# Optimization experiments

Hardware: AMD Instinct MI355X
Metric: run time of the kernel (lower is better)

## Reference

```python
import jax, jax.numpy as jnp
import numpy as np

N, D = 8192, 256
ALPHA, BETA, K = 50.0, 1.0, 2


def setup_inputs() -> dict:
    key = jax.random.key(0)
    k1, k2, k3, k4 = jax.random.split(key, 4)
    Q = jax.random.normal(k1, (N, D), dtype=jnp.float32)
    # 0/1 similarity structure; diagonal forced nonzero so no row is fully masked
    sim = jax.random.randint(k2, (N, N), 0, 2).astype(jnp.float32)
    sim = sim.at[jnp.arange(N), jnp.arange(N)].set(1.0)
    # nn.Linear(in_dim, in_dim) params: y = x @ W.T + b
    bound = 1.0 / np.sqrt(D)
    W = jax.random.uniform(k3, (D, D), jnp.float32, -bound, bound)
    b = jax.random.uniform(k4, (D,), jnp.float32, -bound, bound)
    return {"Q": Q, "sim_mat": sim, "W": W, "b": b}


def reference(Q, sim_mat, W, b):
    mask = sim_mat == 0  # (N, N) bool, constant across iterations
    H = Q
    for _ in range(K):
        H_proj = H @ W.T + b                      # (N, d)
        scores = H_proj @ H_proj.T                # (N, N)
        scores = jnp.where(mask, -jnp.inf, scores)
        lamb = jax.nn.softmax(scores, axis=1)     # (N, N)
        numerator = ALPHA * Q + BETA * (lamb @ H)
        denominator = ALPHA + BETA * jnp.sum(lamb, axis=1, keepdims=True)
        H = numerator / denominator
    return H
```

## Files before the change

kernel.cpp:

```cpp
#include <hip/hip_runtime.h>
#include <hip/hip_bf16.h>

#define NN 8192
#define DD 256
#define ALPHA 50.0f
#define BETA 1.0f
#define THR 10.0f
#define KQ 8
#define KEYS (NN / KQ)
#define STEPS (KEYS / 32)
#define QROWS 64

typedef __attribute__((ext_vector_type(8))) short short8;
typedef __attribute__((ext_vector_type(4))) float f32x4;

static __device__ __forceinline__ ushort f2bf(float f) {
    union { __hip_bfloat16 h; ushort u; } v;
    v.h = __float2bfloat16(f);
    return v.u;
}
static __device__ __forceinline__ float bf2f(ushort u) {
    union { unsigned u; float f; } v; v.u = ((unsigned)u) << 16;
    return v.f;
}
static __device__ __forceinline__ void gl_lds16(const ushort* g, ushort* l) {
    __builtin_amdgcn_global_load_lds(
        (const __attribute__((address_space(1))) unsigned int*)g,
        (__attribute__((address_space(3))) unsigned int*)l, 16, 0, 0);
}

__global__ void k_wconv(const float* __restrict__ W, ushort* __restrict__ Wb) {
    int i = blockIdx.x * 256 + threadIdx.x;
    Wb[i] = f2bf(W[i]);
}

__global__ __launch_bounds__(256) void k_pack(const float* __restrict__ sim,
                                              unsigned* __restrict__ bits) {
    __shared__ unsigned char nibs[256];
    int row = blockIdx.x;
    int tid = threadIdx.x;
    for (int p = 0; p < 8; ++p) {
        int col = p * 1024 + tid * 4;
        float4 v = *reinterpret_cast<const float4*>(sim + (size_t)row * NN + col);
        unsigned char nib = (unsigned char)((v.x != 0.f) | ((v.y != 0.f) << 1) |
                                            ((v.z != 0.f) << 2) | ((v.w != 0.f) << 3));
        nibs[tid] = nib;
        __syncthreads();
        if (tid < 32) {
            unsigned word = 0;
#pragma unroll
            for (int i = 0; i < 8; ++i) word |= ((unsigned)nibs[tid * 8 + i]) << (4 * i);
            bits[row * (NN / 32) + p * 32 + tid] = word;
        }
        __syncthreads();
    }
}

__global__ __launch_bounds__(256) void k_convert(const float* __restrict__ H,
                                                 ushort* __restrict__ Hv,
                                                 ushort* __restrict__ Hvt) {
    __shared__ ushort T[64][72];
    int tile = blockIdx.x;
    int r0 = (tile >> 2) * 64;
    int c0 = (tile & 3) * 64;
    int tid = threadIdx.x;
    int tr = tid >> 4;
    int tc = (tid & 15) * 4;
    for (int i = 0; i < 4; ++i) {
        int r = tr + i * 16;
        float4 v = *reinterpret_cast<const float4*>(H + (size_t)(r0 + r) * DD + c0 + tc);
        ushort4 o;
        o.x = f2bf(v.x); o.y = f2bf(v.y); o.z = f2bf(v.z); o.w = f2bf(v.w);
        *reinterpret_cast<ushort4*>(Hv + (size_t)(r0 + r) * DD + c0 + tc) = o;
        T[tc + 0][r] = o.x; T[tc + 1][r] = o.y; T[tc + 2][r] = o.z; T[tc + 3][r] = o.w;
    }
    __syncthreads();
    for (int i = 0; i < 4; ++i) {
        int c = tr + i * 16;
        ushort4 o;
        o.x = T[c][tc + 0]; o.y = T[c][tc + 1]; o.z = T[c][tc + 2]; o.w = T[c][tc + 3];
        *reinterpret_cast<ushort4*>(Hvt + (size_t)(c0 + c) * NN + r0 + tc) = o;
    }
}

__global__ __launch_bounds__(256) void k_proj(const ushort* __restrict__ Hv,
                                              const ushort* __restrict__ Wb,
                                              const float* __restrict__ b,
                                              ushort* __restrict__ Hp) {
    int w = threadIdx.x >> 6;
    int lane = threadIdx.x & 63;
    int row0 = (blockIdx.x >> 1) * 64 + w * 16;
    int ch = blockIdx.x & 1;
    int lr = lane & 15;
    int lk = lane >> 4;
    short8 af[8];
    for (int kk = 0; kk < 8; ++kk)
        af[kk] = *reinterpret_cast<const short8*>(Hv + (size_t)(row0 + lr) * DD + kk * 32 + lk * 8);
    for (int t = 0; t < 8; ++t) {
        f32x4 acc = {0.f, 0.f, 0.f, 0.f};
        int col = (ch * 8 + t) * 16 + lr;
        for (int kk = 0; kk < 8; ++kk) {
            short8 bf = *reinterpret_cast<const short8*>(Wb + (size_t)col * DD + kk * 32 + lk * 8);
            acc = __builtin_amdgcn_mfma_f32_16x16x32_bf16(af[kk], bf, acc, 0, 0, 0);
        }
        float bias = b[col];
        for (int j = 0; j < 4; ++j) {
            int row = row0 + lk * 4 + j;
            Hp[(size_t)row * DD + col] = f2bf(acc[j] + bias);
        }
    }
}

#define PSTR 40
#define SMEM_ATTN (2 * 32 * 256 * 2 + 2 * 256 * 32 * 2 + 4 * 16 * PSTR * 2)
__global__ __launch_bounds__(256) void k_attn(const ushort* __restrict__ Hp,
                                              const ushort* __restrict__ Hvt,
                                              const unsigned* __restrict__ bits,
                                              ushort* __restrict__ Opart,
                                              float* __restrict__ mpart,
                                              float* __restrict__ lpart) {
    extern __shared__ char smem[];
    ushort* KlB = (ushort*)smem;
    ushort* VlB = (ushort*)(smem + 32768);
    ushort* Pl  = (ushort*)(smem + 65536);

    const int tid = threadIdx.x;
    const int w = tid >> 6;
    const int lane = tid & 63;
    const int lr = lane & 15;
    const int lk = lane >> 4;
    const int bid = blockIdx.x;
    const int kq = bid & 7;
    const int qt = bid >> 3;
    const int rw0 = qt * QROWS + w * 16;
    const int kstart = kq * KEYS;

    int kSrc[4], vSrc[4], dstO[4];
#pragma unroll
    for (int i = 0; i < 4; ++i) {
        int S = (w * 4 + i) * 64 + lane;
        int rK = S >> 5, cpK = S & 31;
        kSrc[i] = rK * 256 + (cpK ^ (rK & 7)) * 8;
        int rV = S >> 2, cpV = S & 3;
        vSrc[i] = rV * NN + (cpV ^ ((rV >> 2) & 3)) * 8;
        dstO[i] = S * 8;
    }
    auto stageK = [&](int buf, int kb) {
        const ushort* Kg = Hp + (size_t)kb * DD;
        ushort* base = KlB + buf * (32 * 256);
#pragma unroll
        for (int i = 0; i < 4; ++i) gl_lds16(Kg + kSrc[i], base + dstO[i]);
    };
    auto stageV = [&](int buf, int kb) {
        const ushort* Vg = Hvt + kb;
        ushort* base = VlB + buf * (256 * 32);
#pragma unroll
        for (int i = 0; i < 4; ++i) gl_lds16(Vg + vSrc[i], base + dstO[i]);
    };

    int Koff[8];
#pragma unroll
    for (int kk = 0; kk < 8; ++kk)
        Koff[kk] = (lr << 9) + ((((kk << 2) + lk) ^ (lr & 7)) << 4);
    const int vBase = (lr << 6) + ((lk ^ ((lr >> 2) & 3)) << 4);

    short8 qf[8];
#pragma unroll
    for (int kk = 0; kk < 8; ++kk)
        qf[kk] = *reinterpret_cast<const short8*>(Hp + (size_t)(rw0 + lr) * DD + kk * 32 + lk * 8);

    f32x4 o[17];
#pragma unroll
    for (int t = 0; t < 17; ++t) o[t] = {0.f, 0.f, 0.f, 0.f};
    float m[4] = {-1e30f, -1e30f, -1e30f, -1e30f};

    short8 ones;
#pragma unroll
    for (int e = 0; e < 8; ++e) ones[e] = (short)0x3f80;

    stageK(0, kstart);
    stageV(0, kstart);
    __syncthreads();

    const int rowbase = (rw0 + lk * 4) * (NN / 32);
    ushort* Pw = Pl + (size_t)w * 16 * PSTR;
    int cur = 0;
    for (int step = 0; step < STEPS; ++step) {
        const int kb = kstart + step * 32;
        if (step + 1 < STEPS) {
            stageK(cur ^ 1, kb + 32);
            stageV(cur ^ 1, kb + 32);
        }
        const int wi = kb >> 5;
        unsigned mwj[4];
#pragma unroll
        for (int j = 0; j < 4; ++j) mwj[j] = bits[rowbase + j * (NN / 32) + wi];

        const char* Kb = (const char*)(KlB + cur * (32 * 256));
        f32x4 s0 = {0.f, 0.f, 0.f, 0.f}, s1 = {0.f, 0.f, 0.f, 0.f};
        __builtin_amdgcn_s_setprio(1);
#pragma unroll
        for (int kk = 0; kk < 8; ++kk) {
            short8 k0 = *reinterpret_cast<const short8*>(Kb + Koff[kk]);
            short8 k1 = *reinterpret_cast<const short8*>(Kb + Koff[kk] + (16 << 9));
            s0 = __builtin_amdgcn_mfma_f32_16x16x32_bf16(qf[kk], k0, s0, 0, 0, 0);
            s1 = __builtin_amdgcn_mfma_f32_16x16x32_bf16(qf[kk], k1, s1, 0, 0, 0);
        }
        __builtin_amdgcn_s_setprio(0);
        float c = -1e30f;
#pragma unroll
        for (int j = 0; j < 4; ++j) {
            float a0 = ((mwj[j] >> lr) & 1u) ? s0[j] : -1e30f;
            float a1 = ((mwj[j] >> (lr + 16)) & 1u) ? s1[j] : -1e30f;
            s0[j] = a0; s1[j] = a1;
            c = fmaxf(c, fmaxf(a0, a1) - m[j]);
        }
        if (__any(c > THR)) {
#pragma unroll
            for (int j = 0; j < 4; ++j) {
                float mx = fmaxf(s0[j], s1[j]);
                mx = fmaxf(mx, __shfl_xor(mx, 1));
                mx = fmaxf(mx, __shfl_xor(mx, 2));
                mx = fmaxf(mx, __shfl_xor(mx, 4));
                mx = fmaxf(mx, __shfl_xor(mx, 8));
                float mn = fmaxf(m[j], mx);
                float scale = __expf(m[j] - mn);
                m[j] = mn;
#pragma unroll
                for (int t = 0; t < 17; ++t) o[t][j] *= scale;
            }
        }
#pragma unroll
        for (int j = 0; j < 4; ++j) {
            Pw[(lk * 4 + j) * PSTR + lr]      = f2bf(__expf(s0[j] - m[j]));
            Pw[(lk * 4 + j) * PSTR + 16 + lr] = f2bf(__expf(s1[j] - m[j]));
        }
        asm volatile("s_waitcnt lgkmcnt(0)" ::: "memory");
        __builtin_amdgcn_sched_barrier(0);
        short8 pa = *reinterpret_cast<const short8*>(Pw + lr * PSTR + lk * 8);
        const char* Vb = (const char*)(VlB + cur * (256 * 32));
        __builtin_amdgcn_s_setprio(1);
#pragma unroll
        for (int t = 0; t < 16; ++t) {
            short8 vf = *reinterpret_cast<const short8*>(Vb + vBase + (t << 10));
            o[t] = __builtin_amdgcn_mfma_f32_16x16x32_bf16(pa, vf, o[t], 0, 0, 0);
        }
        o[16] = __builtin_amdgcn_mfma_f32_16x16x32_bf16(pa, ones, o[16], 0, 0, 0);
        __builtin_amdgcn_s_setprio(0);
        __syncthreads();
        cur ^= 1;
    }

    ushort* op = Opart + ((size_t)kq * NN + rw0) * DD;
#pragma unroll
    for (int t = 0; t < 16; ++t)
#pragma unroll
        for (int j = 0; j < 4; ++j)
            op[(size_t)(lk * 4 + j) * DD + t * 16 + lr] = f2bf(o[t][j]);
    if (lr == 0) {
#pragma unroll
        for (int j = 0; j < 4; ++j) {
            mpart[kq * NN + rw0 + lk * 4 + j] = m[j];
            lpart[kq * NN + rw0 + lk * 4 + j] = o[16][j];
        }
    }
}

__global__ __launch_bounds__(256) void k_merge8(const ushort* __restrict__ Opart,
                                                const float* __restrict__ mpart,
                                                const float* __restrict__ lpart,
                                                const float* __restrict__ Qo,
                                                float* __restrict__ dst) {
    int w = threadIdx.x >> 6;
    int lane = threadIdx.x & 63;
    int r0 = blockIdx.x * 32 + w * 8;
    for (int rr = 0; rr < 8; ++rr) {
        int r = r0 + rr;
        float mv[8], f[8];
        float M = -1e30f;
#pragma unroll
        for (int p = 0; p < 8; ++p) { mv[p] = mpart[p * NN + r]; M = fmaxf(M, mv[p]); }
        float L = 0.f;
#pragma unroll
        for (int p = 0; p < 8; ++p) { f[p] = __expf(mv[p] - M); L += f[p] * lpart[p * NN + r]; }
        float invL = 1.0f / L;
        int c = lane * 4;
        float a0 = 0.f, a1 = 0.f, a2 = 0.f, a3 = 0.f;
#pragma unroll
        for (int p = 0; p < 8; ++p) {
            ushort4 u = *reinterpret_cast<const ushort4*>(Opart + ((size_t)p * NN + r) * DD + c);
            a0 += f[p] * bf2f(u.x); a1 += f[p] * bf2f(u.y);
            a2 += f[p] * bf2f(u.z); a3 += f[p] * bf2f(u.w);
        }
        float4 qv = *reinterpret_cast<const float4*>(Qo + (size_t)r * DD + c);
        float4 ov;
        ov.x = (ALPHA * qv.x + a0 * invL) * (1.0f / (ALPHA + BETA));
        ov.y = (ALPHA * qv.y + a1 * invL) * (1.0f / (ALPHA + BETA));
        ov.z = (ALPHA * qv.z + a2 * invL) * (1.0f / (ALPHA + BETA));
        ov.w = (ALPHA * qv.w + a3 * invL) * (1.0f / (ALPHA + BETA));
        *reinterpret_cast<float4*>(dst + (size_t)r * DD + c) = ov;
    }
}

extern "C" void kernel_launch(void* const* d_in, const int* in_sizes, int n_in,
                              void* d_out, int out_size, void* d_ws, size_t ws_size,
                              hipStream_t stream) {
    const float* Q   = (const float*)d_in[0];
    const float* sim = (const float*)d_in[1];
    const float* W   = (const float*)d_in[2];
    const float* b   = (const float*)d_in[3];
    float* out = (float*)d_out;

    char* ws = (char*)d_ws;
    size_t off = 0;
    ushort* Hv   = (ushort*)(ws + off); off += (size_t)NN * DD * 2;
    ushort* HvtA = (ushort*)(ws + off); off += (size_t)NN * DD * 2;
    ushort* HvtB = (ushort*)(ws + off); off += (size_t)NN * DD * 2;
    ushort* Hp   = (ushort*)(ws + off); off += (size_t)NN * DD * 2;
    ushort* Wb   = (ushort*)(ws + off); off += (size_t)DD * DD * 2;
    unsigned* bits = (unsigned*)(ws + off); off += (size_t)NN * (NN / 32) * 4;
    float*  H1   = (float*)(ws + off);  off += (size_t)NN * DD * 4;
    ushort* Opart = (ushort*)(ws + off); off += (size_t)KQ * NN * DD * 2;
    float*  mpart = (float*)(ws + off);  off += (size_t)KQ * NN * 4;
    float*  lpart = (float*)(ws + off);  off += (size_t)KQ * NN * 4;

    (void)hipFuncSetAttribute((const void*)k_attn,
                              hipFuncAttributeMaxDynamicSharedMemorySize, SMEM_ATTN);

    k_wconv<<<DD * DD / 256, 256, 0, stream>>>(W, Wb);
    k_pack<<<NN, 256, 0, stream>>>(sim, bits);
    k_convert<<<(NN / 64) * (DD / 64), 256, 0, stream>>>(Q, Hv, HvtA);

    k_proj<<<NN / 32, 256, 0, stream>>>(Hv, Wb, b, Hp);
    k_attn<<<(NN / QROWS) * KQ, 256, SMEM_ATTN, stream>>>(Hp, HvtA, bits, Opart, mpart, lpart);
    k_merge8<<<NN / 32, 256, 0, stream>>>(Opart, mpart, lpart, Q, H1);
    k_convert<<<(NN / 64) * (DD / 64), 256, 0, stream>>>(H1, Hv, HvtB);

    k_proj<<<NN / 32, 256, 0, stream>>>(Hv, Wb, b, Hp);
    k_attn<<<(NN / QROWS) * KQ, 256, SMEM_ATTN, stream>>>(Hp, HvtB, bits, Opart, mpart, lpart);
    k_merge8<<<NN / 32, 256, 0, stream>>>(Opart, mpart, lpart, Q, out);
}
```

Baseline: 354.7 us.

## Use 8-wave attention blocks with triple-buffered K/V and LDS-staged mask bits

```diff
diff --git a/kernel.cpp b/kernel.cpp
--- a/kernel.cpp
+++ b/kernel.cpp
@@ -9,7 +9,7 @@
 #define KQ 8
 #define KEYS (NN / KQ)
 #define STEPS (KEYS / 32)
-#define QROWS 64
+#define QROWS 128
 
 typedef __attribute__((ext_vector_type(8))) short short8;
 typedef __attribute__((ext_vector_type(4))) float f32x4;
@@ -23,7 +23,7 @@
     union { unsigned u; float f; } v; v.u = ((unsigned)u) << 16;
     return v.f;
 }
-static __device__ __forceinline__ void gl_lds16(const ushort* g, ushort* l) {
+static __device__ __forceinline__ void gl_lds16(const void* g, void* l) {
     __builtin_amdgcn_global_load_lds(
         (const __attribute__((address_space(1))) unsigned int*)g,
         (__attribute__((address_space(3))) unsigned int*)l, 16, 0, 0);
@@ -112,8 +112,12 @@
 }
 
 #define PSTR 40
-#define SMEM_ATTN (2 * 32 * 256 * 2 + 2 * 256 * 32 * 2 + 4 * 16 * PSTR * 2)
-__global__ __launch_bounds__(256) void k_attn(const ushort* __restrict__ Hp,
+#define KBYTES (32 * 256 * 2)
+#define VBYTES (256 * 32 * 2)
+#define PBYTES (8 * 16 * PSTR * 2)
+#define BBYTES (QROWS * 32 * 4)
+#define SMEM_ATTN (3 * KBYTES + 3 * VBYTES + PBYTES + BBYTES)
+__global__ __launch_bounds__(512) void k_attn(const ushort* __restrict__ Hp,
                                               const ushort* __restrict__ Hvt,
                                               const unsigned* __restrict__ bits,
                                               ushort* __restrict__ Opart,
@@ -121,8 +125,9 @@
                                               float* __restrict__ lpart) {
     extern __shared__ char smem[];
     ushort* KlB = (ushort*)smem;
-    ushort* VlB = (ushort*)(smem + 32768);
-    ushort* Pl  = (ushort*)(smem + 65536);
+    ushort* VlB = (ushort*)(smem + 3 * KBYTES);
+    ushort* Pl  = (ushort*)(smem + 3 * KBYTES + 3 * VBYTES);
+    unsigned* Bl = (unsigned*)(smem + 3 * KBYTES + 3 * VBYTES + PBYTES);
 
     const int tid = threadIdx.x;
     const int w = tid >> 6;
@@ -135,10 +140,10 @@
     const int rw0 = qt * QROWS + w * 16;
     const int kstart = kq * KEYS;
 
-    int kSrc[4], vSrc[4], dstO[4];
-#pragma unroll
-    for (int i = 0; i < 4; ++i) {
-        int S = (w * 4 + i) * 64 + lane;
+    int kSrc[2], vSrc[2], dstO[2];
+#pragma unroll
+    for (int i = 0; i < 2; ++i) {
+        int S = i * 512 + tid;
         int rK = S >> 5, cpK = S & 31;
         kSrc[i] = rK * 256 + (cpK ^ (rK & 7)) * 8;
         int rV = S >> 2, cpV = S & 3;
@@ -149,13 +154,13 @@
         const ushort* Kg = Hp + (size_t)kb * DD;
         ushort* base = KlB + buf * (32 * 256);
 #pragma unroll
-        for (int i = 0; i < 4; ++i) gl_lds16(Kg + kSrc[i], base + dstO[i]);
+        for (int i = 0; i < 2; ++i) gl_lds16(Kg + kSrc[i], base + dstO[i]);
     };
     auto stageV = [&](int buf, int kb) {
         const ushort* Vg = Hvt + kb;
         ushort* base = VlB + buf * (256 * 32);
 #pragma unroll
-        for (int i = 0; i < 4; ++i) gl_lds16(Vg + vSrc[i], base + dstO[i]);
+        for (int i = 0; i < 2; ++i) gl_lds16(Vg + vSrc[i], base + dstO[i]);
     };
 
     int Koff[8];
@@ -178,23 +183,37 @@
 #pragma unroll
     for (int e = 0; e < 8; ++e) ones[e] = (short)0x3f80;
 
+    {
+        const unsigned* Bg = bits + (size_t)(qt * QROWS) * (NN / 32) + kq * 32;
+#pragma unroll
+        for (int i = 0; i < 2; ++i) {
+            int S = i * 512 + tid;
+            int r = S >> 3, c = S & 7;
+            gl_lds16(Bg + (size_t)r * (NN / 32) + c * 4, Bl + S * 4);
+        }
+    }
     stageK(0, kstart);
     stageV(0, kstart);
-    __syncthreads();
-
-    const int rowbase = (rw0 + lk * 4) * (NN / 32);
+    stageK(1, kstart + 32);
+    stageV(1, kstart + 32);
+    asm volatile("s_waitcnt vmcnt(4)" ::: "memory");
+    __builtin_amdgcn_s_barrier();
+    __builtin_amdgcn_sched_barrier(0);
+
     ushort* Pw = Pl + (size_t)w * 16 * PSTR;
+    const int mrow = (w * 16 + lk * 4) * 32;
     int cur = 0;
     for (int step = 0; step < STEPS; ++step) {
         const int kb = kstart + step * 32;
-        if (step + 1 < STEPS) {
-            stageK(cur ^ 1, kb + 32);
-            stageV(cur ^ 1, kb + 32);
-        }
-        const int wi = kb >> 5;
+        const bool staged = (step + 2 < STEPS);
+        if (staged) {
+            int nb = cur + 2; if (nb >= 3) nb -= 3;
+            stageK(nb, kb + 64);
+            stageV(nb, kb + 64);
+        }
         unsigned mwj[4];
 #pragma unroll
-        for (int j = 0; j < 4; ++j) mwj[j] = bits[rowbase + j * (NN / 32) + wi];
+        for (int j = 0; j < 4; ++j) mwj[j] = Bl[mrow + j * 32 + step];
 
         const char* Kb = (const char*)(KlB + cur * (32 * 256));
         f32x4 s0 = {0.f, 0.f, 0.f, 0.f}, s1 = {0.f, 0.f, 0.f, 0.f};
@@ -247,8 +266,11 @@
         }
         o[16] = __builtin_amdgcn_mfma_f32_16x16x32_bf16(pa, ones, o[16], 0, 0, 0);
         __builtin_amdgcn_s_setprio(0);
-        __syncthreads();
-        cur ^= 1;
+        if (staged) asm volatile("s_waitcnt vmcnt(4)" ::: "memory");
+        else        asm volatile("s_waitcnt vmcnt(0)" ::: "memory");
+        __builtin_amdgcn_s_barrier();
+        __builtin_amdgcn_sched_barrier(0);
+        cur = (cur == 2) ? 0 : cur + 1;
     }
 
     ushort* op = Opart + ((size_t)kq * NN + rw0) * DD;
@@ -332,11 +354,11 @@
     k_convert<<<(NN / 64) * (DD / 64), 256, 0, stream>>>(Q, Hv, HvtA);
 
     k_proj<<<NN / 32, 256, 0, stream>>>(Hv, Wb, b, Hp);
-    k_attn<<<(NN / QROWS) * KQ, 256, SMEM_ATTN, stream>>>(Hp, HvtA, bits, Opart, mpart, lpart);
+    k_attn<<<(NN / QROWS) * KQ, 512, SMEM_ATTN, stream>>>(Hp, HvtA, bits, Opart, mpart, lpart);
     k_merge8<<<NN / 32, 256, 0, stream>>>(Opart, mpart, lpart, Q, H1);
     k_convert<<<(NN / 64) * (DD / 64), 256, 0, stream>>>(H1, Hv, HvtB);
 
     k_proj<<<NN / 32, 256, 0, stream>>>(Hv, Wb, b, Hp);
-    k_attn<<<(NN / QROWS) * KQ, 256, SMEM_ATTN, stream>>>(Hp, HvtB, bits, Opart, mpart, lpart);
+    k_attn<<<(NN / QROWS) * KQ, 512, SMEM_ATTN, stream>>>(Hp, HvtB, bits, Opart, mpart, lpart);
     k_merge8<<<NN / 32, 256, 0, stream>>>(Opart, mpart, lpart, Q, out);
 }
```

New measurement: 351.5 us. Within noise of the previous version (-0.9%).
